# Optimization experiments

Measured on AMD Instinct MI355X. Metric: run time of the kernel, lower is better.

Reference implementation:

```python
import jax, jax.numpy as jnp
import numpy as np

C_M, C_Z, C = 256, 128, 32
LN_EPS = 1e-5


def setup_inputs() -> dict:
    key = jax.random.key(0)
    ks = jax.random.split(key, 9)
    S, R = 128, 384  # N_seq, N_res
    m = jax.random.normal(ks[0], (S, R, C_M), dtype=jnp.float32)
    ln_g = jnp.ones((C_M,), jnp.float32)
    ln_b = jnp.zeros((C_M,), jnp.float32)
    w1 = jax.random.normal(ks[1], (C_M, C), jnp.float32) / np.sqrt(C_M)
    b1 = jnp.zeros((C,), jnp.float32)
    w2 = jax.random.normal(ks[2], (C_M, C), jnp.float32) / np.sqrt(C_M)
    b2 = jnp.zeros((C,), jnp.float32)
    w_out = jax.random.normal(ks[3], (C * C, C_Z), jnp.float32) / np.sqrt(C * C)
    b_out = jnp.zeros((C_Z,), jnp.float32)
    return {"m": m, "ln_g": ln_g, "ln_b": ln_b, "w1": w1, "b1": b1,
            "w2": w2, "b2": b2, "w_out": w_out, "b_out": b_out}


def reference(m, ln_g, ln_b, w1, b1, w2, b2, w_out, b_out):
    S, R, _ = m.shape
    # LayerNorm over c_m
    mu = jnp.mean(m, axis=-1, keepdims=True)
    var = jnp.var(m, axis=-1, keepdims=True)
    mn = (m - mu) * jax.lax.rsqrt(var + LN_EPS) * ln_g + ln_b
    a = mn @ w1 + b1  # (S, R, c)
    b = mn @ w2 + b2  # (S, R, c)
    # outer product summed over N_seq: out[i,j,x,y] = sum_s a[s,i,x] b[s,j,y]
    o = jnp.einsum('six,sjy->ijxy', a, b)  # (R, R, c, c)
    o = o.reshape(R, R, C * C) @ w_out + b_out  # (R, R, c_z)
    return o / S
```

## Files before the change

### kernel.cpp

```cpp
#include <hip/hip_runtime.h>
#include <hip/hip_bf16.h>

#define R_RES 384
#define S_SEQ 128
#define CM 256
#define CC 32
#define CZ 128

typedef __attribute__((ext_vector_type(8))) short bf16x8;
typedef __attribute__((ext_vector_type(4))) float f32x4;
typedef __attribute__((ext_vector_type(4))) int i32x4;

__device__ __forceinline__ short tobf16(float f) {
    union { __hip_bfloat16 h; short s; } u;
    u.h = __float2bfloat16(f);
    return u.s;
}

__device__ __forceinline__ void lgkm_barrier() {
    asm volatile("s_waitcnt lgkmcnt(0)" ::: "memory");
    __builtin_amdgcn_s_barrier();
    __builtin_amdgcn_sched_barrier(0);
}

__global__ void k_transpose_wout(const float* __restrict__ w_out, short* __restrict__ wbTf) {
    __shared__ float t[64][65];
    int k0 = blockIdx.x * 64;
    int z0 = blockIdx.y * 64;
    int tid = threadIdx.x;
    int c = tid & 63, rg = tid >> 6;
#pragma unroll
    for (int rr = 0; rr < 16; ++rr) {
        int kk = rg * 16 + rr;
        t[kk][c] = w_out[(size_t)(k0 + kk) * CZ + z0 + c];
    }
    __syncthreads();
#pragma unroll
    for (int l = 0; l < 2; ++l) {
        int id = l * 256 + tid;
        int f = id >> 6;
        int z16l = f >> 1, k32l = f & 1;
        int ln = id & 63;
        int zl = z16l * 16 + (ln & 15);
        int kl = k32l * 32 + (ln >> 4) * 8;
        bf16x8 pk;
#pragma unroll
        for (int j = 0; j < 8; ++j) pk[j] = tobf16(t[kl + j][zl]);
        int z16 = blockIdx.y * 4 + z16l;
        int k32 = blockIdx.x * 2 + k32l;
        *(bf16x8*)(wbTf + ((size_t)(z16 * 32 + k32) * 64 + ln) * 8) = pk;
    }
}

__global__ void k_pack_w12(const float* __restrict__ w1, const float* __restrict__ w2,
                           short* __restrict__ wcT) {
    int idx = blockIdx.x * 256 + threadIdx.x;
    int k = idx >> 6, n = idx & 63;
    float v = (n < 32) ? w1[k * CC + n] : w2[k * CC + (n - 32)];
    wcT[n * CM + k] = tobf16(v);
}

__global__ __launch_bounds__(256) void k_ln_proj(
    const float* __restrict__ M, const float* __restrict__ ln_g, const float* __restrict__ ln_b,
    const float* __restrict__ b1, const float* __restrict__ b2,
    const short* __restrict__ wcT, short* __restrict__ aTf, short* __restrict__ bTf) {
    __shared__ short mnb[64 * 256];
    __shared__ short ab_s[2][32 * 72];
    int r = blockIdx.x >> 1;
    int s0 = (blockIdx.x & 1) * 64;
    int tid = threadIdx.x, lane = tid & 63, w = tid >> 6;
    int g = lane >> 4, r16 = lane & 15;
    float4 gv = *(const float4*)(ln_g + lane * 4);
    float4 bv = *(const float4*)(ln_b + lane * 4);
    for (int it = 0; it < 16; ++it) {
        int sl = it * 4 + w;
        float4 v = *(const float4*)(M + ((size_t)(s0 + sl) * R_RES + r) * CM + lane * 4);
        float sum = v.x + v.y + v.z + v.w;
        float sq = v.x * v.x + v.y * v.y + v.z * v.z + v.w * v.w;
#pragma unroll
        for (int off = 32; off; off >>= 1) {
            sum += __shfl_xor(sum, off);
            sq  += __shfl_xor(sq, off);
        }
        float mu = sum * (1.0f / 256.0f);
        float var = sq * (1.0f / 256.0f) - mu * mu;
        float rstd = rsqrtf(var + 1e-5f);
        short4 mnp;
        mnp.x = tobf16((v.x - mu) * rstd * gv.x + bv.x);
        mnp.y = tobf16((v.y - mu) * rstd * gv.y + bv.y);
        mnp.z = tobf16((v.z - mu) * rstd * gv.z + bv.z);
        mnp.w = tobf16((v.w - mu) * rstd * gv.w + bv.w);
        int byte = sl * 512 + lane * 8;
        byte ^= ((sl & 7) << 4);
        *(short4*)((char*)mnb + byte) = mnp;
    }
    __syncthreads();
    f32x4 acc[4] = {{0,0,0,0},{0,0,0,0},{0,0,0,0},{0,0,0,0}};
    int srow = w * 16 + r16;
#pragma unroll
    for (int ks = 0; ks < 8; ++ks) {
        int byte = srow * 512 + ks * 64 + g * 16;
        byte ^= ((srow & 7) << 4);
        bf16x8 af = *(const bf16x8*)((const char*)mnb + byte);
#pragma unroll
        for (int nt = 0; nt < 4; ++nt) {
            bf16x8 bf = *(const bf16x8*)(wcT + (nt * 16 + r16) * CM + ks * 32 + g * 8);
            acc[nt] = __builtin_amdgcn_mfma_f32_16x16x32_bf16(af, bf, acc[nt], 0, 0, 0);
        }
    }
#pragma unroll
    for (int nt = 0; nt < 4; ++nt) {
        int n = nt * 16 + r16;
        int x = n & 31, sel = n >> 5;
        float bias = sel ? b2[x] : b1[x];
#pragma unroll
        for (int rr = 0; rr < 4; ++rr) {
            int sl = w * 16 + g * 4 + rr;
            ab_s[sel][x * 72 + sl] = tobf16(acc[nt][rr] + bias);
        }
    }
    __syncthreads();
    int piece = tid >> 6;
    int fl = piece >> 1, kl = piece & 1;
    int ln = tid & 63;
    int x = fl * 16 + (ln & 15);
    int s_loc = kl * 32 + (ln >> 4) * 8;
    i32x4 va = *(const i32x4*)((const char*)ab_s[0] + (x * 72 + s_loc) * 2);
    i32x4 vb = *(const i32x4*)((const char*)ab_s[1] + (x * 72 + s_loc) * 2);
    size_t off = ((((size_t)r * 2 + fl) * 4 + (s0 >> 5) + kl) * 64 + ln) * 16;
    *(i32x4*)((char*)aTf + off) = va;
    *(i32x4*)((char*)bTf + off) = vb;
}

__global__ __launch_bounds__(512, 2) void k_opm(
    const short* __restrict__ aTf, const short* __restrict__ bTf,
    const short* __restrict__ wbTf, const float* __restrict__ b_out,
    float* __restrict__ out) {
    __shared__ __align__(16) char smem[114688];
    int tid = threadIdx.x, lane = tid & 63, w = tid >> 6;
    int g = lane >> 4, r16 = lane & 15;
    int wm = w;
    int kh = w & 1, zq = w >> 1;

    bf16x8 wb[2][16];
#pragma unroll
    for (int zt = 0; zt < 2; ++zt)
#pragma unroll
        for (int ks2 = 0; ks2 < 16; ++ks2)
            wb[zt][ks2] = *(const bf16x8*)(wbTf +
                (((size_t)(zq * 2 + zt) * 32 + kh * 16 + ks2) * 64 + lane) * 8);

    int pR = tid >> 5;
    int zR = (tid & 31) * 4;
    float4 bo4 = *(const float4*)(b_out + zR);

    int t0 = blockIdx.x * 18;
    const char* Ab = (const char*)aTf;
    const char* Bb = (const char*)bTf;

    {
        const char* gB = Bb + (size_t)(t0 % 96) * 32768;
#pragma unroll
        for (int q = 0; q < 4; ++q)
            __builtin_amdgcn_global_load_lds(
                (const __attribute__((address_space(1))) void*)(gB + q * 8192 + tid * 16),
                (__attribute__((address_space(3))) void*)(smem + q * 8192 + tid * 16), 16, 0, 0);
    }
    bf16x8 afc = *(const bf16x8*)(Ab + (size_t)((t0 / 96) * 8 + wm) * 4096 + lane * 16);
    asm volatile("s_waitcnt vmcnt(0)" ::: "memory");
    __syncthreads();

    for (int it = 0; it < 18; ++it) {
        int t = t0 + it;
        int bi = t / 96, bj = t % 96;
        int tn = (it < 17) ? t + 1 : t0;
        const char* gAc = Ab + (size_t)(bi * 8 + wm) * 4096;
        const char* gAn = Ab + (size_t)((tn / 96) * 8 + wm) * 4096;
        char* Bcur = smem + (it & 1) * 32768;

        if (it < 17) {
            const char* gB = Bb + (size_t)(tn % 96) * 32768;
            char* Bnxt = smem + ((it + 1) & 1) * 32768;
#pragma unroll
            for (int q = 0; q < 4; ++q)
                __builtin_amdgcn_global_load_lds(
                    (const __attribute__((address_space(1))) void*)(gB + q * 8192 + tid * 16),
                    (__attribute__((address_space(3))) void*)(Bnxt + q * 8192 + tid * 16), 16, 0, 0);
        }

        f32x4 acc[8] = {};
#pragma unroll
        for (int ks = 0; ks < 4; ++ks) {
            bf16x8 bf[8];
#pragma unroll
            for (int ni = 0; ni < 8; ++ni)
                bf[ni] = *(const bf16x8*)(Bcur + ((ni * 4 + ks) * 64 + lane) * 16);
            bf16x8 afn = (ks < 3)
                ? *(const bf16x8*)(gAc + (ks + 1) * 1024 + lane * 16)
                : *(const bf16x8*)(gAn + lane * 16);
            __builtin_amdgcn_s_setprio(1);
#pragma unroll
            for (int ni = 0; ni < 8; ++ni)
                acc[ni] = __builtin_amdgcn_mfma_f32_16x16x32_bf16(bf[ni], afc, acc[ni], 0, 0, 0);
            __builtin_amdgcn_s_setprio(0);
            afc = afn;
        }
        lgkm_barrier();

#pragma unroll
        for (int ni = 0; ni < 8; ++ni) {
            int x = (wm & 1) * 16 + r16;
            int p = (wm >> 1) * 4 + (ni >> 1);
            int y0 = (ni & 1) * 16 + g * 4;
            int byte = (p * 2048 + x * 64 + y0 * 2) ^ (((p & 7) ^ (x & 7)) << 4);
            short4 pk;
            pk.x = tobf16(acc[ni][0]);
            pk.y = tobf16(acc[ni][1]);
            pk.z = tobf16(acc[ni][2]);
            pk.w = tobf16(acc[ni][3]);
            *(short4*)(smem + 65536 + byte) = pk;
        }
        lgkm_barrier();

        f32x4 c0 = {0,0,0,0}, c1 = {0,0,0,0};
#pragma unroll
        for (int ks2 = 0; ks2 < 16; ++ks2) {
            int x = kh * 16 + ks2;
            int abyte = (r16 * 2048 + x * 64 + g * 16) ^ ((((r16 & 7) ^ (x & 7))) << 4);
            bf16x8 a2f = *(const bf16x8*)(smem + 65536 + abyte);
            c0 = __builtin_amdgcn_mfma_f32_16x16x32_bf16(wb[0][ks2], a2f, c0, 0, 0, 0);
            c1 = __builtin_amdgcn_mfma_f32_16x16x32_bf16(wb[1][ks2], a2f, c1, 0, 0, 0);
        }
        {
            int b0 = (kh * 8192 + r16 * 512 + (zq * 32 + g * 4) * 4) ^ ((r16 & 7) << 4);
            int b1 = (kh * 8192 + r16 * 512 + (zq * 32 + 16 + g * 4) * 4) ^ ((r16 & 7) << 4);
            *(f32x4*)(smem + 98304 + b0) = c0;
            *(f32x4*)(smem + 98304 + b1) = c1;
        }
        lgkm_barrier();

        {
            int base = (pR * 512 + zR * 4) ^ ((pR & 7) << 4);
            f32x4 v0 = *(const f32x4*)(smem + 98304 + base);
            f32x4 v1 = *(const f32x4*)(smem + 98304 + 8192 + base);
            f32x4 res;
            res[0] = (v0[0] + v1[0] + bo4.x) * (1.0f / 128.0f);
            res[1] = (v0[1] + v1[1] + bo4.y) * (1.0f / 128.0f);
            res[2] = (v0[2] + v1[2] + bo4.z) * (1.0f / 128.0f);
            res[3] = (v0[3] + v1[3] + bo4.w) * (1.0f / 128.0f);
            int ig = bi * 4 + (pR >> 2);
            int jg = bj * 4 + (pR & 3);
            *(f32x4*)(out + ((size_t)ig * R_RES + jg) * CZ + zR) = res;
        }

        asm volatile("s_waitcnt vmcnt(0)" ::: "memory");
        __syncthreads();
    }
}

extern "C" void kernel_launch(void* const* d_in, const int* in_sizes, int n_in,
                              void* d_out, int out_size, void* d_ws, size_t ws_size,
                              hipStream_t stream) {
    const float* M     = (const float*)d_in[0];
    const float* ln_g  = (const float*)d_in[1];
    const float* ln_b  = (const float*)d_in[2];
    const float* w1    = (const float*)d_in[3];
    const float* b1    = (const float*)d_in[4];
    const float* w2    = (const float*)d_in[5];
    const float* b2    = (const float*)d_in[6];
    const float* w_out = (const float*)d_in[7];
    const float* b_out = (const float*)d_in[8];
    float* out = (float*)d_out;

    short* aTf  = (short*)d_ws;
    short* bTf  = aTf + 12288 * 128;
    short* wbTf = bTf + 12288 * 128;
    short* wcT  = wbTf + 128 * 1024;

    k_transpose_wout<<<dim3(16, 2), 256, 0, stream>>>(w_out, wbTf);
    k_pack_w12<<<64, 256, 0, stream>>>(w1, w2, wcT);
    k_ln_proj<<<768, 256, 0, stream>>>(M, ln_g, ln_b, b1, b2, wcT, aTf, bTf);
    k_opm<<<512, 512, 0, stream>>>(aTf, bTf, wbTf, b_out, out);
}
```

Before: 126.0 us.

## Software-pipeline outer-product and projection GEMMs across tiles with double-buffered LDS

Restructures the OPM kernel so each tile's outer-product MFMAs for tile t+1 are interleaved with the w_out projection MFMAs for tile t. A double-buffered bf16 intermediate in LDS replaces one of the per-tile barrier phases, and B tiles are prefetched two ahead. The grid is halved to 256 blocks of 36 tiles, and LDS grows to 144KB, which likely drops occupancy to one block per CU. The aim is to hide LDS and barrier latency by keeping the matrix units busy, at the cost of more registers and fewer resident waves.

Result: faster. 116.5 us (-7.6%).

```diff
diff --git a/kernel.cpp b/kernel.cpp
--- a/kernel.cpp
+++ b/kernel.cpp
@@ -136,12 +136,29 @@
     const short* __restrict__ aTf, const short* __restrict__ bTf,
     const short* __restrict__ wbTf, const float* __restrict__ b_out,
     float* __restrict__ out) {
-    __shared__ __align__(16) char smem[114688];
+    __shared__ __align__(16) char smem[147456];
     int tid = threadIdx.x, lane = tid & 63, w = tid >> 6;
     int g = lane >> 4, r16 = lane & 15;
     int wm = w;
     int kh = w & 1, zq = w >> 1;
 
+    int t0 = blockIdx.x * 36;
+    const char* Ab = (const char*)aTf;
+    const char* Bb = (const char*)bTf;
+
+    {
+        const char* gB0 = Bb + (size_t)(t0 % 96) * 32768;
+        const char* gB1 = Bb + (size_t)((t0 + 1) % 96) * 32768;
+#pragma unroll
+        for (int q = 0; q < 4; ++q) {
+            __builtin_amdgcn_global_load_lds(
+                (const __attribute__((address_space(1))) void*)(gB0 + q * 8192 + tid * 16),
+                (__attribute__((address_space(3))) void*)(smem + q * 8192 + tid * 16), 16, 0, 0);
+            __builtin_amdgcn_global_load_lds(
+                (const __attribute__((address_space(1))) void*)(gB1 + q * 8192 + tid * 16),
+                (__attribute__((address_space(3))) void*)(smem + 32768 + q * 8192 + tid * 16), 16, 0, 0);
+        }
+    }
     bf16x8 wb[2][16];
 #pragma unroll
     for (int zt = 0; zt < 2; ++zt)
@@ -154,50 +171,22 @@
     int zR = (tid & 31) * 4;
     float4 bo4 = *(const float4*)(b_out + zR);
 
-    int t0 = blockIdx.x * 18;
-    const char* Ab = (const char*)aTf;
-    const char* Bb = (const char*)bTf;
-
-    {
-        const char* gB = Bb + (size_t)(t0 % 96) * 32768;
-#pragma unroll
-        for (int q = 0; q < 4; ++q)
-            __builtin_amdgcn_global_load_lds(
-                (const __attribute__((address_space(1))) void*)(gB + q * 8192 + tid * 16),
-                (__attribute__((address_space(3))) void*)(smem + q * 8192 + tid * 16), 16, 0, 0);
-    }
     bf16x8 afc = *(const bf16x8*)(Ab + (size_t)((t0 / 96) * 8 + wm) * 4096 + lane * 16);
     asm volatile("s_waitcnt vmcnt(0)" ::: "memory");
     __syncthreads();
 
-    for (int it = 0; it < 18; ++it) {
-        int t = t0 + it;
-        int bi = t / 96, bj = t % 96;
-        int tn = (it < 17) ? t + 1 : t0;
-        const char* gAc = Ab + (size_t)(bi * 8 + wm) * 4096;
-        const char* gAn = Ab + (size_t)((tn / 96) * 8 + wm) * 4096;
-        char* Bcur = smem + (it & 1) * 32768;
-
-        if (it < 17) {
-            const char* gB = Bb + (size_t)(tn % 96) * 32768;
-            char* Bnxt = smem + ((it + 1) & 1) * 32768;
-#pragma unroll
-            for (int q = 0; q < 4; ++q)
-                __builtin_amdgcn_global_load_lds(
-                    (const __attribute__((address_space(1))) void*)(gB + q * 8192 + tid * 16),
-                    (__attribute__((address_space(3))) void*)(Bnxt + q * 8192 + tid * 16), 16, 0, 0);
-        }
-
-        f32x4 acc[8] = {};
+    f32x4 acc[8] = {};
+    {
+        const char* gAc = Ab + (size_t)((t0 / 96) * 8 + wm) * 4096;
+        const char* gAn = Ab + (size_t)(((t0 + 1) / 96) * 8 + wm) * 4096;
 #pragma unroll
         for (int ks = 0; ks < 4; ++ks) {
             bf16x8 bf[8];
 #pragma unroll
             for (int ni = 0; ni < 8; ++ni)
-                bf[ni] = *(const bf16x8*)(Bcur + ((ni * 4 + ks) * 64 + lane) * 16);
-            bf16x8 afn = (ks < 3)
-                ? *(const bf16x8*)(gAc + (ks + 1) * 1024 + lane * 16)
-                : *(const bf16x8*)(gAn + lane * 16);
+                bf[ni] = *(const bf16x8*)(smem + ((ni * 4 + ks) * 64 + lane) * 16);
+            bf16x8 afn = (ks < 3) ? *(const bf16x8*)(gAc + (ks + 1) * 1024 + lane * 16)
+                                  : *(const bf16x8*)(gAn + lane * 16);
             __builtin_amdgcn_s_setprio(1);
 #pragma unroll
             for (int ni = 0; ni < 8; ++ni)
@@ -205,51 +194,141 @@
             __builtin_amdgcn_s_setprio(0);
             afc = afn;
         }
-        lgkm_barrier();
-
-#pragma unroll
-        for (int ni = 0; ni < 8; ++ni) {
-            int x = (wm & 1) * 16 + r16;
-            int p = (wm >> 1) * 4 + (ni >> 1);
-            int y0 = (ni & 1) * 16 + g * 4;
-            int byte = (p * 2048 + x * 64 + y0 * 2) ^ (((p & 7) ^ (x & 7)) << 4);
-            short4 pk;
-            pk.x = tobf16(acc[ni][0]);
-            pk.y = tobf16(acc[ni][1]);
-            pk.z = tobf16(acc[ni][2]);
-            pk.w = tobf16(acc[ni][3]);
-            *(short4*)(smem + 65536 + byte) = pk;
-        }
-        lgkm_barrier();
+    }
+    lgkm_barrier();
+#pragma unroll
+    for (int ni = 0; ni < 8; ++ni) {
+        int x = (wm & 1) * 16 + r16;
+        int p = (wm >> 1) * 4 + (ni >> 1);
+        int y0 = (ni & 1) * 16 + g * 4;
+        int byte = (p * 2048 + x * 64 + y0 * 2) ^ (((p & 7) ^ (x & 7)) << 4);
+        short4 pk;
+        pk.x = tobf16(acc[ni][0]);
+        pk.y = tobf16(acc[ni][1]);
+        pk.z = tobf16(acc[ni][2]);
+        pk.w = tobf16(acc[ni][3]);
+        *(short4*)(smem + 65536 + byte) = pk;
+    }
+    lgkm_barrier();
+
+    for (int it = 0; it < 36; ++it) {
+        int t = t0 + it;
+        bool hasN = (it < 35);
+        int tc = t + 1;
+        int tnn = (it < 34) ? t + 2 : t0 + 35;
+
+        if (it < 34) {
+            const char* gB = Bb + (size_t)((t + 2) % 96) * 32768;
+            char* dst = smem + (it & 1) * 32768;
+#pragma unroll
+            for (int q = 0; q < 4; ++q)
+                __builtin_amdgcn_global_load_lds(
+                    (const __attribute__((address_space(1))) void*)(gB + q * 8192 + tid * 16),
+                    (__attribute__((address_space(3))) void*)(dst + q * 8192 + tid * 16), 16, 0, 0);
+        }
+
+        const char* A2r = smem + 65536 + (it & 1) * 32768;
+        const char* Bn  = smem + ((it + 1) & 1) * 32768;
+        const char* gAc = Ab + (size_t)((tc / 96) * 8 + wm) * 4096;
+        const char* gAn = Ab + (size_t)((tnn / 96) * 8 + wm) * 4096;
 
         f32x4 c0 = {0,0,0,0}, c1 = {0,0,0,0};
-#pragma unroll
-        for (int ks2 = 0; ks2 < 16; ++ks2) {
-            int x = kh * 16 + ks2;
-            int abyte = (r16 * 2048 + x * 64 + g * 16) ^ ((((r16 & 7) ^ (x & 7))) << 4);
-            bf16x8 a2f = *(const bf16x8*)(smem + 65536 + abyte);
-            c0 = __builtin_amdgcn_mfma_f32_16x16x32_bf16(wb[0][ks2], a2f, c0, 0, 0, 0);
-            c1 = __builtin_amdgcn_mfma_f32_16x16x32_bf16(wb[1][ks2], a2f, c1, 0, 0, 0);
-        }
+        f32x4 acc2[8] = {};
+#pragma unroll
+        for (int ks = 0; ks < 4; ++ks) {
+            bf16x8 a2f0, a2f1, bfh[4];
+            {
+                int x = kh * 16 + ks * 4 + 0;
+                a2f0 = *(const bf16x8*)(A2r + ((r16 * 2048 + x * 64 + g * 16)
+                        ^ ((((r16 & 7) ^ (x & 7))) << 4)));
+                x = kh * 16 + ks * 4 + 1;
+                a2f1 = *(const bf16x8*)(A2r + ((r16 * 2048 + x * 64 + g * 16)
+                        ^ ((((r16 & 7) ^ (x & 7))) << 4)));
+            }
+            if (hasN) {
+#pragma unroll
+                for (int ni = 0; ni < 4; ++ni)
+                    bfh[ni] = *(const bf16x8*)(Bn + ((ni * 4 + ks) * 64 + lane) * 16);
+            }
+            __builtin_amdgcn_s_setprio(1);
+            c0 = __builtin_amdgcn_mfma_f32_16x16x32_bf16(wb[0][ks * 4 + 0], a2f0, c0, 0, 0, 0);
+            c1 = __builtin_amdgcn_mfma_f32_16x16x32_bf16(wb[1][ks * 4 + 0], a2f0, c1, 0, 0, 0);
+            c0 = __builtin_amdgcn_mfma_f32_16x16x32_bf16(wb[0][ks * 4 + 1], a2f1, c0, 0, 0, 0);
+            c1 = __builtin_amdgcn_mfma_f32_16x16x32_bf16(wb[1][ks * 4 + 1], a2f1, c1, 0, 0, 0);
+            if (hasN) {
+#pragma unroll
+                for (int ni = 0; ni < 4; ++ni)
+                    acc2[ni] = __builtin_amdgcn_mfma_f32_16x16x32_bf16(bfh[ni], afc, acc2[ni], 0, 0, 0);
+            }
+            __builtin_amdgcn_s_setprio(0);
+            bf16x8 a2f2, a2f3;
+            {
+                int x = kh * 16 + ks * 4 + 2;
+                a2f2 = *(const bf16x8*)(A2r + ((r16 * 2048 + x * 64 + g * 16)
+                        ^ ((((r16 & 7) ^ (x & 7))) << 4)));
+                x = kh * 16 + ks * 4 + 3;
+                a2f3 = *(const bf16x8*)(A2r + ((r16 * 2048 + x * 64 + g * 16)
+                        ^ ((((r16 & 7) ^ (x & 7))) << 4)));
+            }
+            if (hasN) {
+#pragma unroll
+                for (int ni = 0; ni < 4; ++ni)
+                    bfh[ni] = *(const bf16x8*)(Bn + (((ni + 4) * 4 + ks) * 64 + lane) * 16);
+            }
+            bf16x8 afn = afc;
+            if (hasN) afn = (ks < 3) ? *(const bf16x8*)(gAc + (ks + 1) * 1024 + lane * 16)
+                                     : *(const bf16x8*)(gAn + lane * 16);
+            __builtin_amdgcn_s_setprio(1);
+            c0 = __builtin_amdgcn_mfma_f32_16x16x32_bf16(wb[0][ks * 4 + 2], a2f2, c0, 0, 0, 0);
+            c1 = __builtin_amdgcn_mfma_f32_16x16x32_bf16(wb[1][ks * 4 + 2], a2f2, c1, 0, 0, 0);
+            c0 = __builtin_amdgcn_mfma_f32_16x16x32_bf16(wb[0][ks * 4 + 3], a2f3, c0, 0, 0, 0);
+            c1 = __builtin_amdgcn_mfma_f32_16x16x32_bf16(wb[1][ks * 4 + 3], a2f3, c1, 0, 0, 0);
+            if (hasN) {
+#pragma unroll
+                for (int ni = 0; ni < 4; ++ni)
+                    acc2[ni + 4] = __builtin_amdgcn_mfma_f32_16x16x32_bf16(bfh[ni], afc, acc2[ni + 4], 0, 0, 0);
+            }
+            __builtin_amdgcn_s_setprio(0);
+            afc = afn;
+        }
+
         {
             int b0 = (kh * 8192 + r16 * 512 + (zq * 32 + g * 4) * 4) ^ ((r16 & 7) << 4);
             int b1 = (kh * 8192 + r16 * 512 + (zq * 32 + 16 + g * 4) * 4) ^ ((r16 & 7) << 4);
-            *(f32x4*)(smem + 98304 + b0) = c0;
-            *(f32x4*)(smem + 98304 + b1) = c1;
+            *(f32x4*)(smem + 131072 + b0) = c0;
+            *(f32x4*)(smem + 131072 + b1) = c1;
         }
         lgkm_barrier();
+
+        if (hasN) {
+            char* A2w = smem + 65536 + ((it + 1) & 1) * 32768;
+#pragma unroll
+            for (int ni = 0; ni < 8; ++ni) {
+                int x = (wm & 1) * 16 + r16;
+                int p = (wm >> 1) * 4 + (ni >> 1);
+                int y0 = (ni & 1) * 16 + g * 4;
+                int byte = (p * 2048 + x * 64 + y0 * 2) ^ (((p & 7) ^ (x & 7)) << 4);
+                short4 pk;
+                pk.x = tobf16(acc2[ni][0]);
+                pk.y = tobf16(acc2[ni][1]);
+                pk.z = tobf16(acc2[ni][2]);
+                pk.w = tobf16(acc2[ni][3]);
+                *(short4*)(A2w + byte) = pk;
+            }
+        }
 
         {
             int base = (pR * 512 + zR * 4) ^ ((pR & 7) << 4);
-            f32x4 v0 = *(const f32x4*)(smem + 98304 + base);
-            f32x4 v1 = *(const f32x4*)(smem + 98304 + 8192 + base);
+            f32x4 v0 = *(const f32x4*)(smem + 131072 + base);
+            f32x4 v1 = *(const f32x4*)(smem + 131072 + 8192 + base);
             f32x4 res;
             res[0] = (v0[0] + v1[0] + bo4.x) * (1.0f / 128.0f);
             res[1] = (v0[1] + v1[1] + bo4.y) * (1.0f / 128.0f);
             res[2] = (v0[2] + v1[2] + bo4.z) * (1.0f / 128.0f);
             res[3] = (v0[3] + v1[3] + bo4.w) * (1.0f / 128.0f);
-            int ig = bi * 4 + (pR >> 2);
-            int jg = bj * 4 + (pR & 3);
+            int bi4 = t / 96, bj4 = t % 96;
+            int ig = bi4 * 4 + (pR >> 2);
+            int jg = bj4 * 4 + (pR & 3);
             *(f32x4*)(out + ((size_t)ig * R_RES + jg) * CZ + zR) = res;
         }
 
@@ -280,5 +359,5 @@
     k_transpose_wout<<<dim3(16, 2), 256, 0, stream>>>(w_out, wbTf);
     k_pack_w12<<<64, 256, 0, stream>>>(w1, w2, wcT);
     k_ln_proj<<<768, 256, 0, stream>>>(M, ln_g, ln_b, b1, b2, wcT, aTf, bTf);
-    k_opm<<<512, 512, 0, stream>>>(aTf, bTf, wbTf, b_out, out);
-}
+    k_opm<<<256, 512, 0, stream>>>(aTf, bTf, wbTf, b_out, out);
+}
```
